# Optimization experiments

Hardware: AMD Instinct MI355X
Metric: run time of the kernel (lower is better)

## Reference

```python
import jax, jax.numpy as jnp
import numpy as np

I, H = 4, 64


def setup_inputs() -> dict:
    key = jax.random.key(0)
    ks = jax.random.split(key, 7)
    s_ih = 1.0 / np.sqrt(H)
    return {
        "x": jax.random.normal(ks[0], (8192, 512, I), dtype=jnp.float32),
        "W_ih": jax.random.uniform(ks[1], (4 * H, I), minval=-s_ih, maxval=s_ih, dtype=jnp.float32),
        "W_hh": jax.random.uniform(ks[2], (4 * H, H), minval=-s_ih, maxval=s_ih, dtype=jnp.float32),
        "b_ih": jax.random.uniform(ks[3], (4 * H,), minval=-s_ih, maxval=s_ih, dtype=jnp.float32),
        "b_hh": jax.random.uniform(ks[4], (4 * H,), minval=-s_ih, maxval=s_ih, dtype=jnp.float32),
        "W_fc": jax.random.uniform(ks[5], (1, H), minval=-s_ih, maxval=s_ih, dtype=jnp.float32),
        "b_fc": jax.random.uniform(ks[6], (1,), minval=-s_ih, maxval=s_ih, dtype=jnp.float32),
    }


def _lstm_last_hidden(x, W_ih, W_hh, b_ih, b_hh):
    # x: [B, T, I] batch_first; PyTorch gate order: i, f, g, o
    B = x.shape[0]
    # Precompute input projections for all timesteps in one GEMM: [T, B, 4H]
    xg = jnp.einsum('bti,gi->tbg', x, W_ih) + (b_ih + b_hh)

    def step(carry, xg_t):
        h, c = carry
        gates = xg_t + h @ W_hh.T  # [B, 4H]
        i, f, g, o = jnp.split(gates, 4, axis=-1)
        i = jax.nn.sigmoid(i)
        f = jax.nn.sigmoid(f)
        g = jnp.tanh(g)
        o = jax.nn.sigmoid(o)
        c = f * c + i * g
        h = o * jnp.tanh(c)
        return (h, c), None

    h0 = jnp.zeros((B, W_hh.shape[1]), dtype=x.dtype)
    c0 = jnp.zeros_like(h0)
    (h_n, _), _ = jax.lax.scan(step, (h0, c0), xg)
    return h_n  # [B, H]


def reference(x, W_ih, W_hh, b_ih, b_hh, W_fc, b_fc):
    h_n = _lstm_last_hidden(x, W_ih, W_hh, b_ih, b_hh)
    return h_n @ W_fc.T + b_fc  # [B, 1]
```

## Files before the change

kernel.cpp:

```cpp
#include <hip/hip_runtime.h>


typedef float f32x4 __attribute__((ext_vector_type(4)));
typedef _Float16 f16x8 __attribute__((ext_vector_type(8)));
typedef _Float16 f16x4 __attribute__((ext_vector_type(4)));

#define TSEQ 512
#define IDIM 4
#define BPB 16
#define TCH 32
#define L2E 1.44269504088896340736f

#if __has_builtin(__builtin_amdgcn_exp2f)
#define EX2(v) __builtin_amdgcn_exp2f(v)
#else
#define EX2(v) exp2f(v)
#endif
#define RCP(v) __builtin_amdgcn_rcpf(v)

__global__ __launch_bounds__(256, 2) void lstm_fused(
    const float* __restrict__ x,
    const float* __restrict__ W_ih,
    const float* __restrict__ W_hh,
    const float* __restrict__ b_ih,
    const float* __restrict__ b_hh,
    const float* __restrict__ W_fc,
    const float* __restrict__ b_fc,
    float* __restrict__ out)
{
    __shared__ __align__(16) _Float16 hbuf[2][BPB * 64];
    __shared__ __align__(8)  f16x4    xstage[BPB * 33];

    const int tid  = threadIdx.x;
    const int lane = tid & 63;
    const int wv   = tid >> 6;
    const int b0   = blockIdx.x * BPB;
    const int r    = lane & 15;
    const int g16  = lane >> 4;

    f16x8 bfrag[4][3];
    float bias[4];
    #pragma unroll
    for (int t4 = 0; t4 < 4; ++t4) {
        const float sc = (t4 == 2) ? 2.0f * L2E : L2E;
        const int g = t4 * 64 + wv * 16 + r;
        #pragma unroll
        for (int ks = 0; ks < 2; ++ks) {
            const float* p = W_hh + g * 64 + ks * 32 + g16 * 8;
            f16x8 f;
            #pragma unroll
            for (int j = 0; j < 8; ++j) f[j] = (_Float16)(p[j] * sc);
            bfrag[t4][ks] = f;
        }
        f16x8 f;
        #pragma unroll
        for (int j = 0; j < 8; ++j) f[j] = (_Float16)0.0f;
        if (g16 == 0) {
            #pragma unroll
            for (int j = 0; j < 4; ++j) f[j] = (_Float16)(W_ih[g * IDIM + j] * sc);
        }
        bfrag[t4][2] = f;
        bias[t4] = (b_ih[g] + b_hh[g]) * sc;
    }
    const float wfc = W_fc[lane];
    const float bfc = b_fc[0];

    float c_reg[4] = {0.f, 0.f, 0.f, 0.f};
    for (int i = tid; i < BPB * 64; i += 256) hbuf[0][i] = (_Float16)0.0f;

    const int bb0 = tid >> 5, tf = tid & 31;
    const float* xg0 = x + ((size_t)(b0 + bb0)     * TSEQ + tf) * IDIM;
    const float* xg1 = x + ((size_t)(b0 + bb0 + 8) * TSEQ + tf) * IDIM;
    float4 xn0 = *(const float4*)xg0;
    float4 xn1 = *(const float4*)xg1;

    const int hbase = r * 128;
    const int hs0 = ((g16 + 0) << 4) ^ ((r & 7) << 4);
    const int hs1 = ((g16 + 4) << 4) ^ ((r & 7) << 4);
    int hw[4];
    #pragma unroll
    for (int q = 0; q < 4; ++q) {
        const int bat = 4 * g16 + q;
        hw[q] = (bat * 128 + (wv * 16 + r) * 2) ^ ((bat & 7) << 4);
    }
    char* hb0 = (char*)&hbuf[0][0];
    char* hb1 = (char*)&hbuf[1][0];

    auto step = [&](int tt, const char* rb, char* wb) {
        f16x8 a0 = *(const f16x8*)(rb + hbase + hs0);
        f16x8 a1 = *(const f16x8*)(rb + hbase + hs1);
        f16x4 xv = f16x4{(_Float16)0.f, (_Float16)0.f, (_Float16)0.f, (_Float16)0.f};
        if (g16 == 0) xv = xstage[r * 33 + tt];
        f16x8 ax;
        ax[0] = xv[0]; ax[1] = xv[1]; ax[2] = xv[2]; ax[3] = xv[3];
        ax[4] = (_Float16)0.f; ax[5] = (_Float16)0.f;
        ax[6] = (_Float16)0.f; ax[7] = (_Float16)0.f;

        f32x4 acc[4];
        __builtin_amdgcn_s_setprio(1);
        #pragma unroll
        for (int t4 = 0; t4 < 4; ++t4) {
            f32x4 a; a[0] = a[1] = a[2] = a[3] = bias[t4];
            a = __builtin_amdgcn_mfma_f32_16x16x32_f16(a0, bfrag[t4][0], a, 0, 0, 0);
            a = __builtin_amdgcn_mfma_f32_16x16x32_f16(a1, bfrag[t4][1], a, 0, 0, 0);
            a = __builtin_amdgcn_mfma_f32_16x16x32_f16(ax, bfrag[t4][2], a, 0, 0, 0);
            acc[t4] = a;
        }
        __builtin_amdgcn_s_setprio(0);

        #pragma unroll
        for (int q = 0; q < 4; ++q) {
            float ei = EX2(-acc[0][q]);
            float ef = EX2(-acc[1][q]);
            float eg = EX2(-acc[2][q]);
            float eo = EX2(-acc[3][q]);
            float ig = (1.f - eg) * RCP((1.f + ei) * (1.f + eg));
            float ff = RCP(1.f + ef);
            float c  = ff * c_reg[q] + ig;
            c_reg[q] = c;
            float uc = fminf(fmaxf(c * (2.0f * L2E), -60.f), 60.f);
            float et = EX2(-uc);
            float h  = (1.f - et) * RCP((1.f + eo) * (1.f + et));
            *(_Float16*)(wb + hw[q]) = (_Float16)h;
        }
        __syncthreads();
    };

    for (int tc = 0; tc < TSEQ; tc += TCH) {
        f16x4 s0, s1;
        s0[0] = (_Float16)xn0.x; s0[1] = (_Float16)xn0.y;
        s0[2] = (_Float16)xn0.z; s0[3] = (_Float16)xn0.w;
        s1[0] = (_Float16)xn1.x; s1[1] = (_Float16)xn1.y;
        s1[2] = (_Float16)xn1.z; s1[3] = (_Float16)xn1.w;
        xstage[bb0 * 33 + tf]       = s0;
        xstage[(bb0 + 8) * 33 + tf] = s1;
        __syncthreads();
        if (tc + TCH < TSEQ) {
            xn0 = *(const float4*)(xg0 + (tc + TCH) * IDIM);
            xn1 = *(const float4*)(xg1 + (tc + TCH) * IDIM);
        }
        for (int tt = 0; tt < TCH; tt += 2) {
            step(tt,     hb0, hb1);
            step(tt + 1, hb1, hb0);
        }
    }

    #pragma unroll
    for (int q = 0; q < 4; ++q) {
        const int bat = 4 * wv + q;
        const int byte = (bat * 128 + lane * 2) ^ ((bat & 7) << 4);
        float hv = (float)*(const _Float16*)(hb0 + byte);
        float partial = hv * wfc;
        #pragma unroll
        for (int off = 32; off > 0; off >>= 1)
            partial += __shfl_down(partial, off);
        if (lane == 0) out[b0 + bat] = partial + bfc;
    }
}

extern "C" void kernel_launch(void* const* d_in, const int* in_sizes, int n_in,
                              void* d_out, int out_size, void* d_ws, size_t ws_size,
                              hipStream_t stream) {
    const float* x    = (const float*)d_in[0];
    const float* W_ih = (const float*)d_in[1];
    const float* W_hh = (const float*)d_in[2];
    const float* b_ih = (const float*)d_in[3];
    const float* b_hh = (const float*)d_in[4];
    const float* W_fc = (const float*)d_in[5];
    const float* b_fc = (const float*)d_in[6];
    float* out = (float*)d_out;

    const int B = in_sizes[0] / (TSEQ * IDIM);
    lstm_fused<<<B / BPB, 256, 0, stream>>>(x, W_ih, W_hh, b_ih, b_hh, W_fc, b_fc, out);
}
```

Before: 330.2 us.

## Precompute next-step input MFMA off critical path, double-buffer x staging

The input-projection MFMA for step t+1 is now issued after the recurrent MFMAs of step t, so the dependent chain per step shrinks from three MFMAs to two. The bias moves into the input fragment as an fp16 hi/lo pair multiplied by constant ones. The x staging buffer is double-buffered and refilled mid-chunk, which removes the extra per-chunk barrier. The cell update is rewritten to use one fewer reciprocal, and __syncthreads is replaced by an explicit lgkmcnt wait plus s_barrier. In exchange, the split fp16 bias adds a little rounding error and more registers are live.

```diff
diff --git a/kernel.cpp b/kernel.cpp
--- a/kernel.cpp
+++ b/kernel.cpp
@@ -9,6 +9,7 @@
 #define IDIM 4
 #define BPB 16
 #define TCH 32
+#define NCH (TSEQ / TCH)
 #define L2E 1.44269504088896340736f
 
 #if __has_builtin(__builtin_amdgcn_exp2f)
@@ -17,6 +18,12 @@
 #define EX2(v) exp2f(v)
 #endif
 #define RCP(v) __builtin_amdgcn_rcpf(v)
+
+#define STEP_BARRIER() do {                                   \
+    asm volatile("s_waitcnt lgkmcnt(0)" ::: "memory");        \
+    __builtin_amdgcn_s_barrier();                             \
+    __builtin_amdgcn_sched_barrier(0);                        \
+} while (0)
 
 __global__ __launch_bounds__(256, 2) void lstm_fused(
     const float* __restrict__ x,
@@ -29,7 +36,7 @@
     float* __restrict__ out)
 {
     __shared__ __align__(16) _Float16 hbuf[2][BPB * 64];
-    __shared__ __align__(8)  f16x4    xstage[BPB * 33];
+    __shared__ __align__(16) f16x4    xstage[2][BPB][33];
 
     const int tid  = threadIdx.x;
     const int lane = tid & 63;
@@ -39,7 +46,6 @@
     const int g16  = lane >> 4;
 
     f16x8 bfrag[4][3];
-    float bias[4];
     #pragma unroll
     for (int t4 = 0; t4 < 4; ++t4) {
         const float sc = (t4 == 2) ? 2.0f * L2E : L2E;
@@ -58,12 +64,16 @@
         if (g16 == 0) {
             #pragma unroll
             for (int j = 0; j < 4; ++j) f[j] = (_Float16)(W_ih[g * IDIM + j] * sc);
+            float biasf = (b_ih[g] + b_hh[g]) * sc;
+            _Float16 hi = (_Float16)biasf;
+            f[4] = hi;
+            f[5] = (_Float16)(biasf - (float)hi);
         }
         bfrag[t4][2] = f;
-        bias[t4] = (b_ih[g] + b_hh[g]) * sc;
     }
     const float wfc = W_fc[lane];
     const float bfc = b_fc[0];
+    const f32x4 zero4 = {0.f, 0.f, 0.f, 0.f};
 
     float c_reg[4] = {0.f, 0.f, 0.f, 0.f};
     for (int i = tid; i < BPB * 64; i += 256) hbuf[0][i] = (_Float16)0.0f;
@@ -73,6 +83,18 @@
     const float* xg1 = x + ((size_t)(b0 + bb0 + 8) * TSEQ + tf) * IDIM;
     float4 xn0 = *(const float4*)xg0;
     float4 xn1 = *(const float4*)xg1;
+    {
+        f16x4 s0, s1;
+        s0[0] = (_Float16)xn0.x; s0[1] = (_Float16)xn0.y;
+        s0[2] = (_Float16)xn0.z; s0[3] = (_Float16)xn0.w;
+        s1[0] = (_Float16)xn1.x; s1[1] = (_Float16)xn1.y;
+        s1[2] = (_Float16)xn1.z; s1[3] = (_Float16)xn1.w;
+        xstage[0][bb0][tf]     = s0;
+        xstage[0][bb0 + 8][tf] = s1;
+    }
+    __syncthreads();
+    xn0 = *(const float4*)(xg0 + TCH * IDIM);
+    xn1 = *(const float4*)(xg1 + TCH * IDIM);
 
     const int hbase = r * 128;
     const int hs0 = ((g16 + 0) << 4) ^ ((r & 7) << 4);
@@ -83,73 +105,98 @@
         const int bat = 4 * g16 + q;
         hw[q] = (bat * 128 + (wv * 16 + r) * 2) ^ ((bat & 7) << 4);
     }
-    char* hb0 = (char*)&hbuf[0][0];
-    char* hb1 = (char*)&hbuf[1][0];
-
-    auto step = [&](int tt, const char* rb, char* wb) {
+    char* hbB = (char*)&hbuf[0][0];
+    const char* xsB = (const char*)&xstage[0][0][0];
+    const int xrow = r * 33 * 8;
+
+    f16x8 axr;
+    axr[4] = (_Float16)1.0f; axr[5] = (_Float16)1.0f;
+    axr[6] = (_Float16)0.0f; axr[7] = (_Float16)0.0f;
+
+    f32x4 accX[4];
+    {
+        f16x4 xv = *(const f16x4*)(xsB + xrow);
+        axr[0] = xv[0]; axr[1] = xv[1]; axr[2] = xv[2]; axr[3] = xv[3];
+        #pragma unroll
+        for (int t4 = 0; t4 < 4; ++t4)
+            accX[t4] = __builtin_amdgcn_mfma_f32_16x16x32_f16(axr, bfrag[t4][2], zero4, 0, 0, 0);
+    }
+
+    auto substep = [&](int t, int P) {
+        const char* rb = hbB + P * 2048;
+        char*       wb = hbB + (P ^ 1) * 2048;
         f16x8 a0 = *(const f16x8*)(rb + hbase + hs0);
         f16x8 a1 = *(const f16x8*)(rb + hbase + hs1);
-        f16x4 xv = f16x4{(_Float16)0.f, (_Float16)0.f, (_Float16)0.f, (_Float16)0.f};
-        if (g16 == 0) xv = xstage[r * 33 + tt];
-        f16x8 ax;
-        ax[0] = xv[0]; ax[1] = xv[1]; ax[2] = xv[2]; ax[3] = xv[3];
-        ax[4] = (_Float16)0.f; ax[5] = (_Float16)0.f;
-        ax[6] = (_Float16)0.f; ax[7] = (_Float16)0.f;
-
-        f32x4 acc[4];
+
+        f32x4 acc2[4];
         __builtin_amdgcn_s_setprio(1);
         #pragma unroll
         for (int t4 = 0; t4 < 4; ++t4) {
-            f32x4 a; a[0] = a[1] = a[2] = a[3] = bias[t4];
-            a = __builtin_amdgcn_mfma_f32_16x16x32_f16(a0, bfrag[t4][0], a, 0, 0, 0);
+            f32x4 a;
+            a = __builtin_amdgcn_mfma_f32_16x16x32_f16(a0, bfrag[t4][0], accX[t4], 0, 0, 0);
             a = __builtin_amdgcn_mfma_f32_16x16x32_f16(a1, bfrag[t4][1], a, 0, 0, 0);
-            a = __builtin_amdgcn_mfma_f32_16x16x32_f16(ax, bfrag[t4][2], a, 0, 0, 0);
-            acc[t4] = a;
+            acc2[t4] = a;
         }
         __builtin_amdgcn_s_setprio(0);
 
+        {
+            const int tb = t + 1;
+            f16x4 xv = *(const f16x4*)(xsB + ((tb >> 5) & 1) * 4224 + xrow + (tb & 31) * 8);
+            axr[0] = xv[0]; axr[1] = xv[1]; axr[2] = xv[2]; axr[3] = xv[3];
+            __builtin_amdgcn_s_setprio(1);
+            #pragma unroll
+            for (int t4 = 0; t4 < 4; ++t4)
+                accX[t4] = __builtin_amdgcn_mfma_f32_16x16x32_f16(axr, bfrag[t4][2], zero4, 0, 0, 0);
+            __builtin_amdgcn_s_setprio(0);
+        }
+
         #pragma unroll
         for (int q = 0; q < 4; ++q) {
-            float ei = EX2(-acc[0][q]);
-            float ef = EX2(-acc[1][q]);
-            float eg = EX2(-acc[2][q]);
-            float eo = EX2(-acc[3][q]);
-            float ig = (1.f - eg) * RCP((1.f + ei) * (1.f + eg));
-            float ff = RCP(1.f + ef);
-            float c  = ff * c_reg[q] + ig;
+            float ei = EX2(-acc2[0][q]);
+            float ef = EX2(-acc2[1][q]);
+            float eg = EX2(-acc2[2][q]);
+            float eo = EX2(-acc2[3][q]);
+            float A  = 1.f + ei, F = 1.f + ef;
+            float Gp = 1.f + eg, Gm = 1.f - eg;
+            float P2  = A * Gp;
+            float num = c_reg[q] * P2 + Gm * F;
+            float c   = num * RCP(P2 * F);
             c_reg[q] = c;
             float uc = fminf(fmaxf(c * (2.0f * L2E), -60.f), 60.f);
             float et = EX2(-uc);
             float h  = (1.f - et) * RCP((1.f + eo) * (1.f + et));
             *(_Float16*)(wb + hw[q]) = (_Float16)h;
         }
-        __syncthreads();
+        STEP_BARRIER();
     };
 
-    for (int tc = 0; tc < TSEQ; tc += TCH) {
-        f16x4 s0, s1;
-        s0[0] = (_Float16)xn0.x; s0[1] = (_Float16)xn0.y;
-        s0[2] = (_Float16)xn0.z; s0[3] = (_Float16)xn0.w;
-        s1[0] = (_Float16)xn1.x; s1[1] = (_Float16)xn1.y;
-        s1[2] = (_Float16)xn1.z; s1[3] = (_Float16)xn1.w;
-        xstage[bb0 * 33 + tf]       = s0;
-        xstage[(bb0 + 8) * 33 + tf] = s1;
-        __syncthreads();
-        if (tc + TCH < TSEQ) {
-            xn0 = *(const float4*)(xg0 + (tc + TCH) * IDIM);
-            xn1 = *(const float4*)(xg1 + (tc + TCH) * IDIM);
-        }
-        for (int tt = 0; tt < TCH; tt += 2) {
-            step(tt,     hb0, hb1);
-            step(tt + 1, hb1, hb0);
-        }
+    for (int t = 0; t < TSEQ; t += 2) {
+        if ((t & (TCH - 1)) == 16) {
+            const int c = t >> 5;
+            if (c + 1 < NCH) {
+                f16x4 s0, s1;
+                s0[0] = (_Float16)xn0.x; s0[1] = (_Float16)xn0.y;
+                s0[2] = (_Float16)xn0.z; s0[3] = (_Float16)xn0.w;
+                s1[0] = (_Float16)xn1.x; s1[1] = (_Float16)xn1.y;
+                s1[2] = (_Float16)xn1.z; s1[3] = (_Float16)xn1.w;
+                f16x4* dst = &xstage[(c + 1) & 1][0][0];
+                dst[bb0 * 33 + tf]       = s0;
+                dst[(bb0 + 8) * 33 + tf] = s1;
+                if (c + 2 < NCH) {
+                    xn0 = *(const float4*)(xg0 + (size_t)(c + 2) * TCH * IDIM);
+                    xn1 = *(const float4*)(xg1 + (size_t)(c + 2) * TCH * IDIM);
+                }
+            }
+        }
+        substep(t,     0);
+        substep(t + 1, 1);
     }
 
     #pragma unroll
     for (int q = 0; q < 4; ++q) {
-        const int bat = 4 * wv + q;
+        const int bat  = wv * 4 + q;
         const int byte = (bat * 128 + lane * 2) ^ ((bat & 7) << 4);
-        float hv = (float)*(const _Float16*)(hb0 + byte);
+        float hv = (float)*(const _Float16*)(hbB + byte);
         float partial = hv * wfc;
         #pragma unroll
         for (int off = 32; off > 0; off >>= 1)
```

Result: slower. 338.7 us (+2.6%).
